# Kernel tuning notes

Measured on AMD Instinct MI355X. Metric: run time of the kernel, lower is better.

The kernel has to match this reference:

```python
import jax, jax.numpy as jnp
import numpy as np

EMBED_DIM = 768
NUM_HEADS = 12
HEAD_DIM = EMBED_DIM // NUM_HEADS


def setup_inputs() -> dict:
    key = jax.random.key(0)
    ks = jax.random.split(key, 5)
    B, N, D = 8, 1024, EMBED_DIM
    s = 1.0 / np.sqrt(D)
    x = jax.random.normal(ks[0], (B, N, D), dtype=jnp.float32)
    W_qkv = jax.random.normal(ks[1], (D, 3 * D), dtype=jnp.float32) * s
    b_qkv = jnp.zeros((3 * D,), dtype=jnp.float32)
    W_proj = jax.random.normal(ks[2], (D, D), dtype=jnp.float32) * s
    b_proj = jnp.zeros((D,), dtype=jnp.float32)
    return {"x": x, "W_qkv": W_qkv, "b_qkv": b_qkv, "W_proj": W_proj, "b_proj": b_proj}


def reference(x, W_qkv, b_qkv, W_proj, b_proj):
    B, N, D = x.shape
    H, Hd = NUM_HEADS, HEAD_DIM
    scale = Hd ** -0.5
    qkv = x @ W_qkv + b_qkv                      # (B, N, 3D)
    qkv = qkv.reshape(B, N, 3, H, Hd).transpose(2, 0, 3, 1, 4)  # (3, B, H, N, Hd)
    q, k, v = qkv[0], qkv[1], qkv[2]
    attn = jnp.einsum('bhnd,bhmd->bhnm', q, k) * scale  # (B, H, N, N)
    attn = jax.nn.softmax(attn, axis=-1)
    out = jnp.einsum('bhnm,bhmd->bhnd', attn, v)        # (B, H, N, Hd)
    out = out.transpose(0, 2, 1, 3).reshape(B, N, D)
    return out @ W_proj + b_proj
```

## Files before the change

### kernel.cpp

```cpp
#include <hip/hip_runtime.h>


#define B_   8
#define N_   1024
#define D_   768
#define H_   12
#define HD_  64

typedef __attribute__((ext_vector_type(4))) float f32x4;
typedef __attribute__((ext_vector_type(8))) short bf16x8;

__device__ __forceinline__ unsigned short f2bf(float f) {
    unsigned int u = __float_as_uint(f);
    u += 0x7fff + ((u >> 16) & 1);
    return (unsigned short)(u >> 16);
}
__device__ __forceinline__ unsigned int pk2(float a, float b) {
    return (unsigned int)f2bf(a) | ((unsigned int)f2bf(b) << 16);
}
__device__ __forceinline__ void gl_lds16(const void* g, void* l) {
    __builtin_amdgcn_global_load_lds(
        (const __attribute__((address_space(1))) unsigned int*)g,
        (__attribute__((address_space(3))) unsigned int*)l, 16, 0, 0);
}
#define MFMA(a, b, c) __builtin_amdgcn_mfma_f32_16x16x32_bf16(a, b, c, 0, 0, 0)

__global__ __launch_bounds__(256) void prep_kernel(
    const float* __restrict__ x, const float* __restrict__ wqkv,
    const float* __restrict__ wproj,
    unsigned short* __restrict__ XB, unsigned short* __restrict__ WQT,
    unsigned short* __restrict__ WPT)
{
    const int bid = blockIdx.x;
    const int tid = threadIdx.x;
    if (bid < 3072) {
        int id = bid * 256 + tid;
        int r  = id & 127;
        int kc = (id >> 7) & 7;
        int ks = (id >> 10) % 12;
        int nt = id / 12288;
        const float* src = x + (size_t)(nt * 128 + r) * 768 + ks * 64 + kc * 8;
        float4 f0 = *(const float4*)src;
        float4 f1 = *(const float4*)(src + 4);
        uint4 o;
        o.x = pk2(f0.x, f0.y); o.y = pk2(f0.z, f0.w);
        o.z = pk2(f1.x, f1.y); o.w = pk2(f1.z, f1.w);
        *(uint4*)&XB[(size_t)id * 8] = o;
    } else if (bid < 3936) {
        int id = (bid - 3072) * 256 + tid;
        int fr = id & 127;
        int kc = (id >> 7) & 7;
        int ks = (id >> 10) % 12;
        int mt = id / 12288;
        float v[8];
#pragma unroll
        for (int j = 0; j < 8; ++j)
            v[j] = wqkv[(size_t)(ks * 64 + kc * 8 + j) * 2304 + mt * 128 + fr];
        uint4 o;
        o.x = pk2(v[0], v[1]); o.y = pk2(v[2], v[3]);
        o.z = pk2(v[4], v[5]); o.w = pk2(v[6], v[7]);
        *(uint4*)&WQT[(size_t)id * 8] = o;
    } else {
        int id = (bid - 3936) * 256 + tid;
        int fr = id & 63;
        int kc = (id >> 6) & 7;
        int ks = (id >> 9) % 12;
        int nt = id / 6144;
        float v[8];
#pragma unroll
        for (int j = 0; j < 8; ++j)
            v[j] = wproj[(size_t)(ks * 64 + kc * 8 + j) * 768 + nt * 64 + fr];
        uint4 o;
        o.x = pk2(v[0], v[1]); o.y = pk2(v[2], v[3]);
        o.z = pk2(v[4], v[5]); o.w = pk2(v[6], v[7]);
        *(uint4*)&WPT[(size_t)id * 8] = o;
    }
}

__global__ __launch_bounds__(256, 3) void qkv_gemm(
    const unsigned short* __restrict__ XB,
    const unsigned short* __restrict__ WQT,
    const float* __restrict__ bias,
    unsigned short* __restrict__ QS,
    unsigned short* __restrict__ KS,
    unsigned short* __restrict__ VS)
{
    __shared__ __align__(16) unsigned short As[8192];
    __shared__ __align__(16) unsigned short Bs[8192];

    const int tid = threadIdx.x;
    const int w = tid >> 6, lane = tid & 63;
    const int l15 = lane & 15, quad = lane >> 4;
    const int mt = blockIdx.x >> 6;
    const int nt = blockIdx.x & 63;
    const int m0w = (w & 1) * 64, n0w = (w >> 1) * 64;

    f32x4 acc[4][4];
    const f32x4 z = {0.f, 0.f, 0.f, 0.f};
#pragma unroll
    for (int t = 0; t < 4; ++t)
#pragma unroll
        for (int u = 0; u < 4; ++u) acc[t][u] = z;

    for (int ks = 0; ks < 12; ++ks) {
        const char* slabA = (const char*)(WQT + (size_t)(mt * 12 + ks) * 8192);
        const char* slabB = (const char*)(XB  + (size_t)(nt * 12 + ks) * 8192);
#pragma unroll
        for (int i = 0; i < 4; ++i) {
            const int c = (w * 4 + i);
            gl_lds16(slabA + (c * 64 + lane) * 16, (char*)As + c * 1024);
            gl_lds16(slabB + (c * 64 + lane) * 16, (char*)Bs + c * 1024);
        }
        __syncthreads();
#pragma unroll
        for (int kk = 0; kk < 2; ++kk) {
            bf16x8 af[4], bfv[4];
#pragma unroll
            for (int t = 0; t < 4; ++t)
                af[t] = *(const bf16x8*)(As + (((kk * 4 + quad) * 128) + m0w + t * 16 + l15) * 8);
#pragma unroll
            for (int u = 0; u < 4; ++u)
                bfv[u] = *(const bf16x8*)(Bs + (((kk * 4 + quad) * 128) + n0w + u * 16 + l15) * 8);
#pragma unroll
            for (int t = 0; t < 4; ++t)
#pragma unroll
                for (int u = 0; u < 4; ++u)
                    acc[t][u] = MFMA(af[t], bfv[u], acc[t][u]);
        }
        __syncthreads();
    }

    const int part = mt / 6;
#pragma unroll
    for (int t = 0; t < 4; ++t) {
        int flocal = (mt % 6) * 128 + m0w + t * 16 + quad * 4;
        float4 bv = *(const float4*)&bias[part * 768 + flocal];
        int h = flocal >> 6, d0 = flocal & 63;
#pragma unroll
        for (int u = 0; u < 4; ++u) {
            int token = nt * 128 + n0w + u * 16 + l15;
            int b = token >> 10, n = token & 1023;
            int bh = b * H_ + h;
            f32x4 a = acc[t][u];
            float v0 = a[0] + bv.x, v1 = a[1] + bv.y;
            float v2 = a[2] + bv.z, v3 = a[3] + bv.w;
            if (part == 0) {
                int qt = n >> 7, r = n & 127;
                size_t idx = ((size_t)(bh * 8 + qt) * 1024 + (d0 >> 3) * 128 + r) * 8 + (d0 & 7);
                uint2 pp; pp.x = pk2(v0, v1); pp.y = pk2(v2, v3);
                *(uint2*)&QS[idx] = pp;
            } else if (part == 1) {
                int kt = n >> 6, r = n & 63;
                size_t idx = ((size_t)(bh * 16 + kt) * 512 + (d0 >> 3) * 64 + r) * 8 + (d0 & 7);
                uint2 pp; pp.x = pk2(v0, v1); pp.y = pk2(v2, v3);
                *(uint2*)&KS[idx] = pp;
            } else {
                int kt = n >> 6, r = n & 63;
                size_t base = ((size_t)(bh * 16 + kt) * 512 + (r >> 3) * 64 + d0) * 8 + (r & 7);
                VS[base]      = f2bf(v0);
                VS[base + 8]  = f2bf(v1);
                VS[base + 16] = f2bf(v2);
                VS[base + 24] = f2bf(v3);
            }
        }
    }
}

__global__ __launch_bounds__(256, 3) void attn_kernel(
    const unsigned short* __restrict__ QS,
    const unsigned short* __restrict__ KS,
    const unsigned short* __restrict__ VS,
    unsigned short* __restrict__ AWS)
{
    __shared__ __align__(16) unsigned short Qs[8192];
    __shared__ __align__(16) unsigned short Ks[4096];
    __shared__ __align__(16) unsigned short Vs[4096];

    const int tid = threadIdx.x;
    const int w = tid >> 6, lane = tid & 63;
    const int l15 = lane & 15, quad = lane >> 4;
    const int bh = blockIdx.x % 96;
    const int qt = blockIdx.x / 96;
    const float C = 0.18033688f;

    const char* qslab = (const char*)(QS + (size_t)(bh * 8 + qt) * 8192);
#pragma unroll
    for (int i = 0; i < 4; ++i) {
        const int c = w * 4 + i;
        gl_lds16(qslab + (c * 64 + lane) * 16, (char*)Qs + c * 1024);
    }
    __syncthreads();
    bf16x8 qf[2][2];
#pragma unroll
    for (int u = 0; u < 2; ++u)
#pragma unroll
        for (int s = 0; s < 2; ++s)
            qf[u][s] = *(const bf16x8*)(Qs + ((s * 4 + quad) * 128 + w * 32 + u * 16 + l15) * 8);

    f32x4 o[4][2];
    const f32x4 z = {0.f, 0.f, 0.f, 0.f};
#pragma unroll
    for (int t = 0; t < 4; ++t) { o[t][0] = z; o[t][1] = z; }
    float lsum[2] = {0.f, 0.f};

    for (int kt = 0; kt < 16; ++kt) {
        const char* kslab = (const char*)(KS + (size_t)(bh * 16 + kt) * 4096);
        const char* vslab = (const char*)(VS + (size_t)(bh * 16 + kt) * 4096);
        __syncthreads();
#pragma unroll
        for (int i = 0; i < 2; ++i) {
            const int c = w * 2 + i;
            gl_lds16(kslab + (c * 64 + lane) * 16, (char*)Ks + c * 1024);
            gl_lds16(vslab + (c * 64 + lane) * 16, (char*)Vs + c * 1024);
        }
        __syncthreads();

        f32x4 s[4][2];
#pragma unroll
        for (int t = 0; t < 4; ++t) { s[t][0] = z; s[t][1] = z; }
#pragma unroll
        for (int ss = 0; ss < 2; ++ss) {
            bf16x8 kf[4];
#pragma unroll
            for (int t = 0; t < 4; ++t)
                kf[t] = *(const bf16x8*)(Ks + ((ss * 4 + quad) * 64 + t * 16 + l15) * 8);
#pragma unroll
            for (int t = 0; t < 4; ++t)
#pragma unroll
                for (int u = 0; u < 2; ++u)
                    s[t][u] = MFMA(kf[t], qf[u][ss], s[t][u]);
        }

        unsigned int pkk[2][4][2];
#pragma unroll
        for (int u = 0; u < 2; ++u) {
#pragma unroll
            for (int t = 0; t < 4; ++t) {
                float p0 = __builtin_amdgcn_exp2f(s[t][u][0] * C);
                float p1 = __builtin_amdgcn_exp2f(s[t][u][1] * C);
                float p2 = __builtin_amdgcn_exp2f(s[t][u][2] * C);
                float p3 = __builtin_amdgcn_exp2f(s[t][u][3] * C);
                lsum[u] += (p0 + p1) + (p2 + p3);
                pkk[u][t][0] = pk2(p0, p1);
                pkk[u][t][1] = pk2(p2, p3);
            }
        }

#pragma unroll
        for (int ss = 0; ss < 2; ++ss) {
            unsigned int bfr[2][4];
#pragma unroll
            for (int u = 0; u < 2; ++u)
#pragma unroll
                for (int jj = 0; jj < 4; ++jj) {
                    int sq = (quad & 1) * 2 + (jj >> 1);
                    int src = l15 + sq * 16;
                    int v0 = __shfl((int)pkk[u][2 * ss][jj & 1], src, 64);
                    int v1 = __shfl((int)pkk[u][2 * ss + 1][jj & 1], src, 64);
                    bfr[u][jj] = (quad >> 1) ? (unsigned int)v1 : (unsigned int)v0;
                }
            bf16x8 vf[4];
#pragma unroll
            for (int t = 0; t < 4; ++t)
                vf[t] = *(const bf16x8*)(Vs + ((ss * 4 + quad) * 64 + t * 16 + l15) * 8);
#pragma unroll
            for (int u = 0; u < 2; ++u) {
                union { unsigned int uu[4]; bf16x8 v; } cv;
                cv.uu[0] = bfr[u][0]; cv.uu[1] = bfr[u][1];
                cv.uu[2] = bfr[u][2]; cv.uu[3] = bfr[u][3];
#pragma unroll
                for (int t = 0; t < 4; ++t)
                    o[t][u] = MFMA(vf[t], cv.v, o[t][u]);
            }
        }
    }

    float inv[2];
#pragma unroll
    for (int u = 0; u < 2; ++u) {
        float l = lsum[u];
        l += __shfl_xor(l, 16, 64);
        l += __shfl_xor(l, 32, 64);
        inv[u] = 1.f / l;
    }
    const int b = bh / H_, h = bh % H_;
    const int mt = b * 8 + qt;
#pragma unroll
    for (int t = 0; t < 4; ++t) {
        int d0 = t * 16 + quad * 4;
#pragma unroll
        for (int u = 0; u < 2; ++u) {
            int ql = w * 32 + u * 16 + l15;
            size_t idx = ((size_t)(mt * 12 + h) * 1024 + (d0 >> 3) * 128 + ql) * 8 + (d0 & 7);
            uint2 pp;
            pp.x = pk2(o[t][u][0] * inv[u], o[t][u][1] * inv[u]);
            pp.y = pk2(o[t][u][2] * inv[u], o[t][u][3] * inv[u]);
            *(uint2*)&AWS[idx] = pp;
        }
    }
}

__global__ __launch_bounds__(256, 3) void proj_gemm(
    const unsigned short* __restrict__ AWS,
    const unsigned short* __restrict__ WPT,
    const float* __restrict__ bias, float* __restrict__ out)
{
    __shared__ __align__(16) unsigned short As[8192];
    __shared__ __align__(16) unsigned short Bs[4096];

    const int tid = threadIdx.x;
    const int w = tid >> 6, lane = tid & 63;
    const int l15 = lane & 15, quad = lane >> 4;
    const int mt = blockIdx.x / 12;
    const int nt = blockIdx.x % 12;
    const int m0w = (w & 1) * 64, n0w = (w >> 1) * 32;

    f32x4 acc[4][2];
    const f32x4 z = {0.f, 0.f, 0.f, 0.f};
#pragma unroll
    for (int t = 0; t < 4; ++t) { acc[t][0] = z; acc[t][1] = z; }

    for (int ks = 0; ks < 12; ++ks) {
        const char* slabA = (const char*)(AWS + (size_t)(mt * 12 + ks) * 8192);
        const char* slabB = (const char*)(WPT + (size_t)(nt * 12 + ks) * 4096);
#pragma unroll
        for (int i = 0; i < 4; ++i) {
            const int c = w * 4 + i;
            gl_lds16(slabA + (c * 64 + lane) * 16, (char*)As + c * 1024);
        }
#pragma unroll
        for (int i = 0; i < 2; ++i) {
            const int c = w * 2 + i;
            gl_lds16(slabB + (c * 64 + lane) * 16, (char*)Bs + c * 1024);
        }
        __syncthreads();
#pragma unroll
        for (int kk = 0; kk < 2; ++kk) {
            bf16x8 af[4], bfv[2];
#pragma unroll
            for (int t = 0; t < 4; ++t)
                af[t] = *(const bf16x8*)(As + (((kk * 4 + quad) * 128) + m0w + t * 16 + l15) * 8);
#pragma unroll
            for (int u = 0; u < 2; ++u)
                bfv[u] = *(const bf16x8*)(Bs + (((kk * 4 + quad) * 64) + n0w + u * 16 + l15) * 8);
#pragma unroll
            for (int t = 0; t < 4; ++t)
#pragma unroll
                for (int u = 0; u < 2; ++u)
                    acc[t][u] = MFMA(af[t], bfv[u], acc[t][u]);
        }
        __syncthreads();
    }

#pragma unroll
    for (int t = 0; t < 4; ++t)
#pragma unroll
        for (int u = 0; u < 2; ++u) {
            int col = nt * 64 + n0w + u * 16 + l15;
            float bvv = bias[col];
#pragma unroll
            for (int r = 0; r < 4; ++r) {
                int row = mt * 128 + m0w + t * 16 + quad * 4 + r;
                out[(size_t)row * 768 + col] = acc[t][u][r] + bvv;
            }
        }
}

extern "C" void kernel_launch(void* const* d_in, const int* in_sizes, int n_in,
                              void* d_out, int out_size, void* d_ws, size_t ws_size,
                              hipStream_t stream) {
    const float* x     = (const float*)d_in[0];
    const float* Wqkv  = (const float*)d_in[1];
    const float* bqkv  = (const float*)d_in[2];
    const float* Wproj = (const float*)d_in[3];
    const float* bproj = (const float*)d_in[4];
    float* out = (float*)d_out;

    unsigned short* ws = (unsigned short*)d_ws;
    unsigned short* XB  = ws;
    unsigned short* WQT = ws + 6291456;
    unsigned short* WPT = ws + 8060928;
    unsigned short* QS  = ws + 8650752;
    unsigned short* KS  = ws + 14942208;
    unsigned short* VS  = ws + 21233664;
    unsigned short* AWS = ws + 27525120;

    prep_kernel<<<dim3(4224), dim3(256), 0, stream>>>(x, Wqkv, Wproj, XB, WQT, WPT);
    qkv_gemm<<<dim3(18 * 64), dim3(256), 0, stream>>>(XB, WQT, bqkv, QS, KS, VS);
    attn_kernel<<<dim3(96 * 8), dim3(256), 0, stream>>>(QS, KS, VS, AWS);
    proj_gemm<<<dim3(64 * 12), dim3(256), 0, stream>>>(AWS, WPT, bproj, out);
}
```

Measured before the change: 202.2 us.

## Double-buffer LDS tiles with async prefetch in all three GEMM/attention kernels

Adds double-buffered LDS staging to the QKV GEMM, attention and projection kernels. The next tile's global-to-LDS loads are issued before computing on the current tile, with explicit vmcnt waits and raw barriers, so memory latency overlaps MFMA work. The QKV GEMM now uses half-depth k-slices (24 steps) to keep LDS per block the same, and its occupancy hint rises to 4. The softmax probabilities are truncated to bf16 instead of rounded, using a byte-perm pack to save ALU work at a slight accuracy cost.

```diff
diff --git a/kernel.cpp b/kernel.cpp
--- a/kernel.cpp
+++ b/kernel.cpp
@@ -18,12 +18,24 @@
 __device__ __forceinline__ unsigned int pk2(float a, float b) {
     return (unsigned int)f2bf(a) | ((unsigned int)f2bf(b) << 16);
 }
+__device__ __forceinline__ unsigned int pk2t(float a, float b) {
+    return __builtin_amdgcn_perm(__float_as_uint(b), __float_as_uint(a), 0x07060302u);
+}
+__device__ __forceinline__ float truncbf(float f) {
+    return __uint_as_float(__float_as_uint(f) & 0xFFFF0000u);
+}
 __device__ __forceinline__ void gl_lds16(const void* g, void* l) {
     __builtin_amdgcn_global_load_lds(
         (const __attribute__((address_space(1))) unsigned int*)g,
         (__attribute__((address_space(3))) unsigned int*)l, 16, 0, 0);
 }
 #define MFMA(a, b, c) __builtin_amdgcn_mfma_f32_16x16x32_bf16(a, b, c, 0, 0, 0)
+#define BAR() do { __asm__ volatile("" ::: "memory"); \
+    __builtin_amdgcn_s_barrier(); \
+    __asm__ volatile("" ::: "memory"); } while (0)
+#define WAITVM(n) do { __asm__ volatile("" ::: "memory"); \
+    __builtin_amdgcn_s_waitcnt(0xF70 | (n)); \
+    __asm__ volatile("" ::: "memory"); } while (0)
 
 __global__ __launch_bounds__(256) void prep_kernel(
     const float* __restrict__ x, const float* __restrict__ wqkv,
@@ -77,7 +89,7 @@
     }
 }
 
-__global__ __launch_bounds__(256, 3) void qkv_gemm(
+__global__ __launch_bounds__(256, 4) void qkv_gemm(
     const unsigned short* __restrict__ XB,
     const unsigned short* __restrict__ WQT,
     const float* __restrict__ bias,
@@ -85,8 +97,8 @@
     unsigned short* __restrict__ KS,
     unsigned short* __restrict__ VS)
 {
-    __shared__ __align__(16) unsigned short As[8192];
-    __shared__ __align__(16) unsigned short Bs[8192];
+    __shared__ __align__(16) unsigned short As[2][4096];
+    __shared__ __align__(16) unsigned short Bs[2][4096];
 
     const int tid = threadIdx.x;
     const int w = tid >> 6, lane = tid & 63;
@@ -95,6 +107,21 @@
     const int nt = blockIdx.x & 63;
     const int m0w = (w & 1) * 64, n0w = (w >> 1) * 64;
 
+    const char* baseA = (const char*)(WQT + (size_t)(mt * 12) * 8192);
+    const char* baseB = (const char*)(XB  + (size_t)(nt * 12) * 8192);
+
+    auto issue = [&](int ks) {
+        const char* sA = baseA + ks * 8192;
+        const char* sB = baseB + ks * 8192;
+        const int pb = ks & 1;
+#pragma unroll
+        for (int i = 0; i < 2; ++i) {
+            const int c = w * 2 + i;
+            gl_lds16(sA + (c * 64 + lane) * 16, (char*)As + pb * 8192 + c * 1024);
+            gl_lds16(sB + (c * 64 + lane) * 16, (char*)Bs + pb * 8192 + c * 1024);
+        }
+    };
+
     f32x4 acc[4][4];
     const f32x4 z = {0.f, 0.f, 0.f, 0.f};
 #pragma unroll
@@ -102,32 +129,25 @@
 #pragma unroll
         for (int u = 0; u < 4; ++u) acc[t][u] = z;
 
-    for (int ks = 0; ks < 12; ++ks) {
-        const char* slabA = (const char*)(WQT + (size_t)(mt * 12 + ks) * 8192);
-        const char* slabB = (const char*)(XB  + (size_t)(nt * 12 + ks) * 8192);
-#pragma unroll
-        for (int i = 0; i < 4; ++i) {
-            const int c = (w * 4 + i);
-            gl_lds16(slabA + (c * 64 + lane) * 16, (char*)As + c * 1024);
-            gl_lds16(slabB + (c * 64 + lane) * 16, (char*)Bs + c * 1024);
-        }
-        __syncthreads();
-#pragma unroll
-        for (int kk = 0; kk < 2; ++kk) {
-            bf16x8 af[4], bfv[4];
-#pragma unroll
-            for (int t = 0; t < 4; ++t)
-                af[t] = *(const bf16x8*)(As + (((kk * 4 + quad) * 128) + m0w + t * 16 + l15) * 8);
+    issue(0);
+    for (int ks = 0; ks < 24; ++ks) {
+        BAR();
+        if (ks < 23) { issue(ks + 1); WAITVM(4); } else { WAITVM(0); }
+        BAR();
+        const unsigned short* Ab = As[ks & 1];
+        const unsigned short* Bb = Bs[ks & 1];
+        bf16x8 af[4], bfv[4];
+#pragma unroll
+        for (int t = 0; t < 4; ++t)
+            af[t] = *(const bf16x8*)(Ab + (quad * 128 + m0w + t * 16 + l15) * 8);
+#pragma unroll
+        for (int u = 0; u < 4; ++u)
+            bfv[u] = *(const bf16x8*)(Bb + (quad * 128 + n0w + u * 16 + l15) * 8);
+#pragma unroll
+        for (int t = 0; t < 4; ++t)
 #pragma unroll
             for (int u = 0; u < 4; ++u)
-                bfv[u] = *(const bf16x8*)(Bs + (((kk * 4 + quad) * 128) + n0w + u * 16 + l15) * 8);
-#pragma unroll
-            for (int t = 0; t < 4; ++t)
-#pragma unroll
-                for (int u = 0; u < 4; ++u)
-                    acc[t][u] = MFMA(af[t], bfv[u], acc[t][u]);
-        }
-        __syncthreads();
+                acc[t][u] = MFMA(af[t], bfv[u], acc[t][u]);
     }
 
     const int part = mt / 6;
@@ -173,8 +193,8 @@
     unsigned short* __restrict__ AWS)
 {
     __shared__ __align__(16) unsigned short Qs[8192];
-    __shared__ __align__(16) unsigned short Ks[4096];
-    __shared__ __align__(16) unsigned short Vs[4096];
+    __shared__ __align__(16) unsigned short Ks[2][4096];
+    __shared__ __align__(16) unsigned short Vs[2][4096];
 
     const int tid = threadIdx.x;
     const int w = tid >> 6, lane = tid & 63;
@@ -183,13 +203,31 @@
     const int qt = blockIdx.x / 96;
     const float C = 0.18033688f;
 
+    const char* kbase = (const char*)(KS + (size_t)(bh * 16) * 4096);
+    const char* vbase = (const char*)(VS + (size_t)(bh * 16) * 4096);
+
+    auto issue_tile = [&](int kt) {
+        const char* ks_ = kbase + kt * 8192;
+        const char* vs_ = vbase + kt * 8192;
+        const int pb = kt & 1;
+#pragma unroll
+        for (int i = 0; i < 2; ++i) {
+            const int c = w * 2 + i;
+            gl_lds16(ks_ + (c * 64 + lane) * 16, (char*)Ks + pb * 8192 + c * 1024);
+            gl_lds16(vs_ + (c * 64 + lane) * 16, (char*)Vs + pb * 8192 + c * 1024);
+        }
+    };
+
     const char* qslab = (const char*)(QS + (size_t)(bh * 8 + qt) * 8192);
 #pragma unroll
     for (int i = 0; i < 4; ++i) {
         const int c = w * 4 + i;
         gl_lds16(qslab + (c * 64 + lane) * 16, (char*)Qs + c * 1024);
     }
-    __syncthreads();
+    issue_tile(0);
+
+    WAITVM(4);
+    BAR();
     bf16x8 qf[2][2];
 #pragma unroll
     for (int u = 0; u < 2; ++u)
@@ -204,16 +242,11 @@
     float lsum[2] = {0.f, 0.f};
 
     for (int kt = 0; kt < 16; ++kt) {
-        const char* kslab = (const char*)(KS + (size_t)(bh * 16 + kt) * 4096);
-        const char* vslab = (const char*)(VS + (size_t)(bh * 16 + kt) * 4096);
-        __syncthreads();
-#pragma unroll
-        for (int i = 0; i < 2; ++i) {
-            const int c = w * 2 + i;
-            gl_lds16(kslab + (c * 64 + lane) * 16, (char*)Ks + c * 1024);
-            gl_lds16(vslab + (c * 64 + lane) * 16, (char*)Vs + c * 1024);
-        }
-        __syncthreads();
+        BAR();
+        if (kt < 15) { issue_tile(kt + 1); WAITVM(4); } else { WAITVM(0); }
+        BAR();
+        const unsigned short* Kb = Ks[kt & 1];
+        const unsigned short* Vb = Vs[kt & 1];
 
         f32x4 s[4][2];
 #pragma unroll
@@ -223,7 +256,7 @@
             bf16x8 kf[4];
 #pragma unroll
             for (int t = 0; t < 4; ++t)
-                kf[t] = *(const bf16x8*)(Ks + ((ss * 4 + quad) * 64 + t * 16 + l15) * 8);
+                kf[t] = *(const bf16x8*)(Kb + ((ss * 4 + quad) * 64 + t * 16 + l15) * 8);
 #pragma unroll
             for (int t = 0; t < 4; ++t)
 #pragma unroll
@@ -236,13 +269,13 @@
         for (int u = 0; u < 2; ++u) {
 #pragma unroll
             for (int t = 0; t < 4; ++t) {
-                float p0 = __builtin_amdgcn_exp2f(s[t][u][0] * C);
-                float p1 = __builtin_amdgcn_exp2f(s[t][u][1] * C);
-                float p2 = __builtin_amdgcn_exp2f(s[t][u][2] * C);
-                float p3 = __builtin_amdgcn_exp2f(s[t][u][3] * C);
+                float p0 = truncbf(__builtin_amdgcn_exp2f(s[t][u][0] * C));
+                float p1 = truncbf(__builtin_amdgcn_exp2f(s[t][u][1] * C));
+                float p2 = truncbf(__builtin_amdgcn_exp2f(s[t][u][2] * C));
+                float p3 = truncbf(__builtin_amdgcn_exp2f(s[t][u][3] * C));
                 lsum[u] += (p0 + p1) + (p2 + p3);
-                pkk[u][t][0] = pk2(p0, p1);
-                pkk[u][t][1] = pk2(p2, p3);
+                pkk[u][t][0] = pk2t(p0, p1);
+                pkk[u][t][1] = pk2t(p2, p3);
             }
         }
 
@@ -262,7 +295,7 @@
             bf16x8 vf[4];
 #pragma unroll
             for (int t = 0; t < 4; ++t)
-                vf[t] = *(const bf16x8*)(Vs + ((ss * 4 + quad) * 64 + t * 16 + l15) * 8);
+                vf[t] = *(const bf16x8*)(Vb + ((ss * 4 + quad) * 64 + t * 16 + l15) * 8);
 #pragma unroll
             for (int u = 0; u < 2; ++u) {
                 union { unsigned int uu[4]; bf16x8 v; } cv;
@@ -305,8 +338,8 @@
     const unsigned short* __restrict__ WPT,
     const float* __restrict__ bias, float* __restrict__ out)
 {
-    __shared__ __align__(16) unsigned short As[8192];
-    __shared__ __align__(16) unsigned short Bs[4096];
+    __shared__ __align__(16) unsigned short As[2][8192];
+    __shared__ __align__(16) unsigned short Bs[2][4096];
 
     const int tid = threadIdx.x;
     const int w = tid >> 6, lane = tid & 63;
@@ -315,41 +348,52 @@
     const int nt = blockIdx.x % 12;
     const int m0w = (w & 1) * 64, n0w = (w >> 1) * 32;
 
+    const char* baseA = (const char*)(AWS + (size_t)(mt * 12) * 8192);
+    const char* baseB = (const char*)(WPT + (size_t)(nt * 12) * 4096);
+
+    auto issue = [&](int ks) {
+        const char* sA = baseA + ks * 16384;
+        const char* sB = baseB + ks * 8192;
+        const int pb = ks & 1;
+#pragma unroll
+        for (int i = 0; i < 4; ++i) {
+            const int c = w * 4 + i;
+            gl_lds16(sA + (c * 64 + lane) * 16, (char*)As + pb * 16384 + c * 1024);
+        }
+#pragma unroll
+        for (int i = 0; i < 2; ++i) {
+            const int c = w * 2 + i;
+            gl_lds16(sB + (c * 64 + lane) * 16, (char*)Bs + pb * 8192 + c * 1024);
+        }
+    };
+
     f32x4 acc[4][2];
     const f32x4 z = {0.f, 0.f, 0.f, 0.f};
 #pragma unroll
     for (int t = 0; t < 4; ++t) { acc[t][0] = z; acc[t][1] = z; }
 
+    issue(0);
     for (int ks = 0; ks < 12; ++ks) {
-        const char* slabA = (const char*)(AWS + (size_t)(mt * 12 + ks) * 8192);
-        const char* slabB = (const char*)(WPT + (size_t)(nt * 12 + ks) * 4096);
-#pragma unroll
-        for (int i = 0; i < 4; ++i) {
-            const int c = w * 4 + i;
-            gl_lds16(slabA + (c * 64 + lane) * 16, (char*)As + c * 1024);
-        }
-#pragma unroll
-        for (int i = 0; i < 2; ++i) {
-            const int c = w * 2 + i;
-            gl_lds16(slabB + (c * 64 + lane) * 16, (char*)Bs + c * 1024);
-        }
-        __syncthreads();
+        BAR();
+        if (ks < 11) { issue(ks + 1); WAITVM(6); } else { WAITVM(0); }
+        BAR();
+        const unsigned short* Ab = As[ks & 1];
+        const unsigned short* Bb = Bs[ks & 1];
 #pragma unroll
         for (int kk = 0; kk < 2; ++kk) {
             bf16x8 af[4], bfv[2];
 #pragma unroll
             for (int t = 0; t < 4; ++t)
-                af[t] = *(const bf16x8*)(As + (((kk * 4 + quad) * 128) + m0w + t * 16 + l15) * 8);
+                af[t] = *(const bf16x8*)(Ab + (((kk * 4 + quad) * 128) + m0w + t * 16 + l15) * 8);
 #pragma unroll
             for (int u = 0; u < 2; ++u)
-                bfv[u] = *(const bf16x8*)(Bs + (((kk * 4 + quad) * 64) + n0w + u * 16 + l15) * 8);
+                bfv[u] = *(const bf16x8*)(Bb + (((kk * 4 + quad) * 64) + n0w + u * 16 + l15) * 8);
 #pragma unroll
             for (int t = 0; t < 4; ++t)
 #pragma unroll
                 for (int u = 0; u < 2; ++u)
                     acc[t][u] = MFMA(af[t], bfv[u], acc[t][u]);
         }
-        __syncthreads();
     }
 
 #pragma unroll
```

Result: faster. 194.2 us (-4.0%).
